# Optimization experiments

Measured on AMD Instinct MI355X. Metric: run time of the kernel, lower is better.

Reference implementation:

```python
import jax, jax.numpy as jnp
import numpy as np

LMAX, MMAX = 4, 2
L1 = LMAX + 1                      # 5 coefficients with m=0
NL = [LMAX + 1 - m for m in range(MMAX + 1)]   # [5,4,3] degrees per |m|
K = (LMAX + 1) ** 2                # 25 full SH coefficients
KR = NL[0] + 2 * sum(NL[1:])       # 19 coefficients with |m|<=mmax
# degree l of each row in the reduced (m-primary) layout:
# m=0: l=0..4 | m=+1: l=1..4 | m=-1: l=1..4 | m=+2: l=2..4 | m=-2: l=2..4
L_IDX = np.array([0,1,2,3,4, 1,2,3,4, 1,2,3,4, 2,3,4, 2,3,4])


def so2_conv(x, rad, w0, b0, wr1, wi1, wr2, wi2, c_out, extra):
    """SO(2)-equivariant conv over m-primary layout x: [E, KR, c_in].
    rad: optional per-edge radial weights [E, sum_m nl_m*c_in]."""
    E, _, c_in = x.shape
    # m = 0 block
    x0 = x[:, :L1].reshape(E, L1 * c_in)
    if rad is not None:
        x0 = x0 * rad[:, :L1 * c_in]
    y0 = x0 @ w0 + b0
    out0 = y0[:, :L1 * c_out].reshape(E, L1, c_out)
    gating = y0[:, L1 * c_out:] if extra else None
    outs = [out0]
    off_x, off_r = L1, L1 * c_in
    for nl, wr, wi in ((NL[1], wr1, wi1), (NL[2], wr2, wi2)):
        xr = x[:, off_x:off_x + nl].reshape(E, nl * c_in)
        xi = x[:, off_x + nl:off_x + 2 * nl].reshape(E, nl * c_in)
        if rad is not None:
            rm = rad[:, off_r:off_r + nl * c_in]
            xr, xi = xr * rm, xi * rm
        yr = xr @ wr - xi @ wi   # complex-style SO2 mixing
        yi = xi @ wr + xr @ wi
        outs += [yr.reshape(E, nl, c_out), yi.reshape(E, nl, c_out)]
        off_x += 2 * nl
        off_r += nl * c_in
    return jnp.concatenate(outs, axis=1), gating


def gate_act(gating, x):
    """GateActivation: silu on l=0 scalars, sigmoid gates per degree l>=1."""
    E, _, H = x.shape
    g = jax.nn.sigmoid(gating).reshape(E, LMAX, H)
    g_ext = jnp.concatenate([jnp.ones((E, 1, H), x.dtype), g], axis=1)
    out = x * g_ext[:, L_IDX]           # l=0 row gated by 1, replaced below
    return out.at[:, 0].set(jax.nn.silu(x[:, 0]))


def setup_inputs() -> dict:
    key = jax.random.key(0)
    ks = jax.random.split(key, 32)
    E, N, C, H, D, RH = 50000, 2500, 64, 64, 128, 64
    c_in1 = 2 * C
    rad_dim = sum(nl * c_in1 for nl in NL)          # 1536
    extra = LMAX * H                                 # 256

    def w(k, shape):
        return jax.random.normal(k, shape, jnp.float32) / np.sqrt(shape[0])

    inp = {
        'node_feats': jax.random.normal(ks[0], (N, K, C), jnp.float32),
        'edge_embeds': jax.random.normal(ks[1], (E, D), jnp.float32),
        'wigner': jax.random.normal(ks[2], (E, KR, K), jnp.float32) / np.sqrt(K),
        'wigner_inv': jax.random.normal(ks[3], (E, K, KR), jnp.float32) / np.sqrt(KR),
        'edge_envelope': jax.random.uniform(ks[4], (E, 1, 1), jnp.float32),
        'rad_w1': w(ks[5], (D, RH)), 'rad_b1': jnp.zeros((RH,), jnp.float32),
        'rad_w2': w(ks[6], (RH, rad_dim)), 'rad_b2': jnp.zeros((rad_dim,), jnp.float32),
        'w1_m0': w(ks[7], (L1 * c_in1, L1 * H + extra)),
        'b1_m0': jnp.zeros((L1 * H + extra,), jnp.float32),
        'w1_r1': w(ks[8], (NL[1] * c_in1, NL[1] * H)),
        'w1_i1': w(ks[9], (NL[1] * c_in1, NL[1] * H)),
        'w1_r2': w(ks[10], (NL[2] * c_in1, NL[2] * H)),
        'w1_i2': w(ks[11], (NL[2] * c_in1, NL[2] * H)),
        'w2_m0': w(ks[12], (L1 * H, L1 * C)),
        'b2_m0': jnp.zeros((L1 * C,), jnp.float32),
        'w2_r1': w(ks[13], (NL[1] * H, NL[1] * C)),
        'w2_i1': w(ks[14], (NL[1] * H, NL[1] * C)),
        'w2_r2': w(ks[15], (NL[2] * H, NL[2] * C)),
        'w2_i2': w(ks[16], (NL[2] * H, NL[2] * C)),
        'senders': jax.random.randint(ks[17], (E,), 0, N, jnp.int32),
        'receivers': jax.random.randint(ks[18], (E,), 0, N, jnp.int32),
    }
    return inp


def reference(node_feats, edge_embeds, wigner, wigner_inv, edge_envelope,
              rad_w1, rad_b1, rad_w2, rad_b2,
              w1_m0, b1_m0, w1_r1, w1_i1, w1_r2, w1_i2,
              w2_m0, b2_m0, w2_r1, w2_i1, w2_r2, w2_i2,
              senders, receivers):
    num_nodes = node_feats.shape[0]
    C = node_feats.shape[2]
    H = w2_m0.shape[0] // L1
    # gather + concat: [E, K, 2C]
    msg = jnp.concatenate((node_feats[senders], node_feats[receivers]), axis=2)
    # rotate to edge frame, truncated to |m|<=mmax: [E, KR, 2C]
    msg = jnp.einsum('erk,ekc->erc', wigner, msg)
    # per-edge radial weights for conv1
    rad = jax.nn.silu(edge_embeds @ rad_w1 + rad_b1) @ rad_w2 + rad_b2
    msg, gating = so2_conv(msg, rad, w1_m0, b1_m0, w1_r1, w1_i1, w1_r2, w1_i2,
                           c_out=H, extra=LMAX * H)
    msg = gate_act(gating, msg)
    msg, _ = so2_conv(msg, None, w2_m0, b2_m0, w2_r1, w2_i1, w2_r2, w2_i2,
                      c_out=C, extra=0)
    msg = msg * edge_envelope
    # rotate back to global frame: [E, K, C]
    msg = jnp.einsum('ekr,erc->ekc', wigner_inv, msg)
    return jax.ops.segment_sum(msg, receivers, num_segments=num_nodes)
```

## Files before the change

kernel.cpp:

```cpp
#include <hip/hip_runtime.h>


typedef __attribute__((ext_vector_type(8))) short bf16x8;
typedef __attribute__((ext_vector_type(4))) float f32x4;

union U8 { uint4 v; unsigned short s[8]; };

__device__ __forceinline__ unsigned short f2b(float f) {
    unsigned u = __float_as_uint(f);
    unsigned r = (u + 0x7FFFu + ((u >> 16) & 1u)) >> 16;
    return (unsigned short)r;
}
__device__ __forceinline__ float b2f(unsigned short h) {
    return __uint_as_float(((unsigned)h) << 16);
}
__device__ __forceinline__ float sigm_(float x){ return 1.0f/(1.0f+__expf(-x)); }
__device__ __forceinline__ float silu_(float x){ return x/(1.0f+__expf(-x)); }

#define OFF_W1T   0L
#define OFF_W1C1  409600L
#define OFF_W1C2  933888L
#define OFF_V0T   1327104L
#define OFF_V1C   1449984L
#define OFF_V2C   1712128L
#define OFF_RW2T  1908736L
#define W_TOTAL   2007040L
#define NNODES    2500
#define NFT_ELEMS (2500L * 2048L)

__global__ void k_prep(const float* __restrict__ w1m0, const float* __restrict__ w1r1,
                       const float* __restrict__ w1i1, const float* __restrict__ w1r2,
                       const float* __restrict__ w1i2, const float* __restrict__ w2m0,
                       const float* __restrict__ w2r1, const float* __restrict__ w2i1,
                       const float* __restrict__ w2r2, const float* __restrict__ w2i2,
                       const float* __restrict__ rw2, short* __restrict__ W)
{
    long i = (long)blockIdx.x * blockDim.x + threadIdx.x;
    if (i >= W_TOTAL) return;
    float v;
    if (i < OFF_W1C1) {
        int n = (int)(i / 640), k = (int)(i % 640);
        v = (n < 576) ? w1m0[k * 576 + n] : 0.f;
    } else if (i < OFF_W1C2) {
        long j = i - OFF_W1C1; int n = (int)(j >> 10), k = (int)(j & 1023);
        v = (n < 256) ? ((k < 512) ? w1r1[k*256 + n] : -w1i1[(k-512)*256 + n])
                      : ((k < 512) ? w1i1[k*256 + (n-256)] : w1r1[(k-512)*256 + (n-256)]);
    } else if (i < OFF_V0T) {
        long j = i - OFF_W1C2; int n = (int)(j / 768), k = (int)(j % 768);
        v = (n >= 384) ? 0.f
          : (n < 192) ? ((k < 384) ? w1r2[k*192 + n] : -w1i2[(k-384)*192 + n])
                      : ((k < 384) ? w1i2[k*192 + (n-192)] : w1r2[(k-384)*192 + (n-192)]);
    } else if (i < OFF_V1C) {
        long j = i - OFF_V0T; int n = (int)(j / 320), k = (int)(j % 320);
        v = (n < 320) ? w2m0[k * 320 + n] : 0.f;
    } else if (i < OFF_V2C) {
        long j = i - OFF_V1C; int n = (int)(j >> 9), k = (int)(j & 511);
        v = (n < 256) ? ((k < 256) ? w2r1[k*256 + n] : -w2i1[(k-256)*256 + n])
                      : ((k < 256) ? w2i1[k*256 + (n-256)] : w2r1[(k-256)*256 + (n-256)]);
    } else if (i < OFF_RW2T) {
        long j = i - OFF_V2C; int n = (int)(j / 384), k = (int)(j % 384);
        v = (n >= 384) ? 0.f
          : (n < 192) ? ((k < 192) ? w2r2[k*192 + n] : -w2i2[(k-192)*192 + n])
                      : ((k < 192) ? w2i2[k*192 + (n-192)] : w2r2[(k-192)*192 + (n-192)]);
    } else {
        long j = i - OFF_RW2T; int n = (int)(j >> 6), d = (int)(j & 63);
        v = rw2[d * 1536 + n];
    }
    W[i] = (short)f2b(v);
}

__global__ __launch_bounds__(256)
void k_nft(const float* __restrict__ nf, short* __restrict__ nfT)
{
    __shared__ float s_nf[25 * 65];
    const int t = threadIdx.x;
    const long nn = blockIdx.x;
    for (int p = t; p < 1600; p += 256) {
        int r = p >> 6, c = p & 63;
        s_nf[r * 65 + c] = nf[nn * 1600 + p];
    }
    __syncthreads();
    for (int i = t; i < 2048; i += 256) {
        int c = i >> 5, k = i & 31;
        float v = (k < 25) ? s_nf[k * 65 + c] : 0.f;
        nfT[nn * 2048 + i] = (short)f2b(v);
    }
}

__global__ void k_hist(const int* __restrict__ rcv, int* __restrict__ cnt, long e0, long n)
{
    long e = (long)blockIdx.x * 256 + threadIdx.x;
    if (e < n) atomicAdd(&cnt[rcv[e0 + e]], 1);
}

__global__ __launch_bounds__(256)
void k_scan(const int* __restrict__ cnt, int* __restrict__ off, int* __restrict__ nxt)
{
    __shared__ int part[256];
    const int t = threadIdx.x;
    const int base = t * 10;
    int loc[10]; int s = 0;
    #pragma unroll
    for (int j = 0; j < 10; ++j) {
        int idx = base + j;
        int v = (idx < NNODES) ? cnt[idx] : 0;
        loc[j] = s; s += v;
    }
    part[t] = s;
    __syncthreads();
    for (int d = 1; d < 256; d <<= 1) {
        int v = part[t];
        int u = (t >= d) ? part[t - d] : 0;
        __syncthreads();
        part[t] = v + u;
        __syncthreads();
    }
    int excl = (t == 0) ? 0 : part[t - 1];
    #pragma unroll
    for (int j = 0; j < 10; ++j) {
        int idx = base + j;
        if (idx < NNODES) { int o = excl + loc[j]; off[idx] = o; nxt[idx] = o; }
    }
}

__global__ void k_scat(const int* __restrict__ rcv, int* __restrict__ nxt,
                       int* __restrict__ perm, long e0, long n)
{
    long e = (long)blockIdx.x * 256 + threadIdx.x;
    if (e < n) {
        int p = atomicAdd(&nxt[rcv[e0 + e]], 1);
        perm[p] = (int)e;
    }
}

__global__ __launch_bounds__(512)
void k_rad(const float* __restrict__ ee, const float* __restrict__ rw1,
           const float* __restrict__ rb1, const float* __restrict__ rb2,
           const short* __restrict__ RW2T, short* __restrict__ rad,
           long e0, long Etot)
{
    __shared__ __align__(16) short s_h[32 * 64];
    const int t = threadIdx.x, w = t >> 6, l = t & 63, l15 = l & 15, lhi = l >> 4;
    const long eb = (long)blockIdx.x * 32;

    #pragma unroll
    for (int j = 0; j < 4; ++j) {
        int i = t + j * 512;
        int e = i >> 6, d = i & 63;
        long ge = e0 + eb + e;
        float a = rb1[d];
        if (ge < Etot) {
            const float* ep = ee + ge * 128;
            #pragma unroll 16
            for (int dd = 0; dd < 128; ++dd) a = fmaf(ep[dd], rw1[dd * 64 + d], a);
            a = silu_(a);
        } else a = 0.f;
        *(short*)((char*)s_h + e * 128 + ((d * 2) ^ ((e & 7) << 4))) = (short)f2b(a);
    }
    __syncthreads();

    f32x4 acc[6][2][2];
    #pragma unroll
    for (int g = 0; g < 6; ++g)
        #pragma unroll
        for (int mt = 0; mt < 2; ++mt)
            #pragma unroll
            for (int nt = 0; nt < 2; ++nt)
                acc[g][mt][nt] = (f32x4){0.f, 0.f, 0.f, 0.f};

    #pragma unroll
    for (int ks = 0; ks < 2; ++ks) {
        bf16x8 af[2];
        #pragma unroll
        for (int mt = 0; mt < 2; ++mt)
            af[mt] = *(const bf16x8*)((const char*)s_h + (mt * 16 + l15) * 128 +
                                      (((ks << 6) + (lhi << 4)) ^ ((l & 7) << 4)));
        #pragma unroll
        for (int g = 0; g < 6; ++g) {
            int grp = w + g * 8;
            #pragma unroll
            for (int nt = 0; nt < 2; ++nt) {
                int col = grp * 32 + nt * 16 + l15;
                bf16x8 bf = *(const bf16x8*)(RW2T + (long)col * 64 + (ks << 5) + (lhi << 3));
                #pragma unroll
                for (int mt = 0; mt < 2; ++mt)
                    acc[g][mt][nt] = __builtin_amdgcn_mfma_f32_16x16x32_bf16(af[mt], bf, acc[g][mt][nt], 0, 0, 0);
            }
        }
    }
    #pragma unroll
    for (int g = 0; g < 6; ++g)
        #pragma unroll
        for (int nt = 0; nt < 2; ++nt) {
            int col = (w + g * 8) * 32 + nt * 16 + l15;
            float bias = rb2[col];
            #pragma unroll
            for (int mt = 0; mt < 2; ++mt)
                #pragma unroll
                for (int r = 0; r < 4; ++r) {
                    int e = mt * 16 + lhi * 4 + r;
                    rad[(eb + e) * 1536 + col] = (short)f2b(acc[g][mt][nt][r] + bias);
                }
        }
}

__global__ __launch_bounds__(256)
void k_rot2(const float* __restrict__ wig, const short* __restrict__ nfT,
            const short* __restrict__ rad,
            const int* __restrict__ snd, const int* __restrict__ rcv,
            short* __restrict__ X, long e0, long nchunk)
{
    __shared__ float s_wg[4][480];
    __shared__ __align__(16) short s_rot[4][20 * 128];
    const int t = threadIdx.x, w = t >> 6, l = t & 63, l15 = l & 15, lhi = l >> 4;
    const long eb = (long)blockIdx.x * 4;
    const long el = eb + w;
    const bool valid = (el < nchunk);

    for (int p = t; p < 4 * 475; p += 256) {
        int e = p / 475, q = p - e * 475;
        if (eb + e < nchunk) s_wg[e][q] = wig[(e0 + eb + e) * 475 + q];
    }
    __syncthreads();

    if (valid) {
        long ge = e0 + el;
        int n0 = snd[ge], n1 = rcv[ge];
        U8 a0u, a1u;
        #pragma unroll
        for (int j = 0; j < 8; ++j) {
            int k = lhi * 8 + j;
            a0u.s[j] = (k < 25) ? f2b(s_wg[w][l15 * 25 + k]) : (unsigned short)0;
            a1u.s[j] = (l15 < 3 && k < 25) ? f2b(s_wg[w][(16 + l15) * 25 + k]) : (unsigned short)0;
        }
        bf16x8 a0 = *(bf16x8*)&a0u, a1 = *(bf16x8*)&a1u;

        f32x4 acc0[8], acc1[8];
        #pragma unroll
        for (int nt = 0; nt < 8; ++nt) {
            acc0[nt] = (f32x4){0.f, 0.f, 0.f, 0.f};
            acc1[nt] = (f32x4){0.f, 0.f, 0.f, 0.f};
        }
        #pragma unroll
        for (int nt = 0; nt < 8; ++nt) {
            int col = nt * 16 + l15;
            bf16x8 b = *(const bf16x8*)(nfT + (long)(col < 64 ? n0 : n1) * 2048 +
                                        (long)(col & 63) * 32 + (lhi << 3));
            acc0[nt] = __builtin_amdgcn_mfma_f32_16x16x32_bf16(a0, b, acc0[nt], 0, 0, 0);
            acc1[nt] = __builtin_amdgcn_mfma_f32_16x16x32_bf16(a1, b, acc1[nt], 0, 0, 0);
        }
        char* base = (char*)s_rot[w];
        #pragma unroll
        for (int nt = 0; nt < 8; ++nt) {
            int col2 = (nt * 16 + l15) * 2;
            #pragma unroll
            for (int r = 0; r < 4; ++r) {
                int row = lhi * 4 + r;
                *(short*)(base + ((row * 256 + col2) ^ ((row & 7) << 4))) = (short)f2b(acc0[nt][r]);
            }
            if (lhi == 0) {
                #pragma unroll
                for (int r = 0; r < 4; ++r) {
                    int row = 16 + r;
                    *(short*)(base + ((row * 256 + col2) ^ ((row & 7) << 4))) = (short)f2b(acc1[nt][r]);
                }
            }
        }
    }
    __syncthreads();

    short* xp = X + el * 2432;
    if (valid) {
        const short* rp = rad + el * 1536;
        #pragma unroll
        for (int it = 0; it < 5; ++it) {
            int q = l + it * 64;
            if (q < 304) {
                int r = q >> 4, c0 = (q & 15) << 3;
                int rr = (r < 9) ? r : ((r < 16) ? r - 4 : r - 7);
                U8 rot; rot.v = *(uint4*)((char*)s_rot[w] + ((r * 256 + c0 * 2) ^ ((r & 7) << 4)));
                U8 rd;  rd.v  = *(const uint4*)(rp + rr * 128 + c0);
                U8 o;
                #pragma unroll
                for (int j = 0; j < 8; ++j) o.s[j] = f2b(b2f(rot.s[j]) * b2f(rd.s[j]));
                *(uint4*)(xp + q * 8) = o.v;
            }
        }
    } else {
        #pragma unroll
        for (int it = 0; it < 5; ++it) {
            int q = l + it * 64;
            if (q < 304) *(uint4*)(xp + q * 8) = (uint4){0, 0, 0, 0};
        }
    }
}

template<int Km, int Nreal, int GMODE, int EPI>
__device__ __forceinline__ void gemm_body(
    const short* __restrict__ A, const long RS, const int gofs,
    const short* __restrict__ W, const float* __restrict__ bias,
    short* __restrict__ O, const long OS, const int oofs,
    short* __restrict__ sA, short* __restrict__ sB, const int et, const int cb)
{
    const int t = threadIdx.x, w = t >> 6, l = t & 63, l15 = l & 15, lhi = l >> 4;
    const long eb = (long)et * 128;
    const short* Ap = A + eb * RS;
    const short* Wp = W + (long)cb * Km;

    f32x4 acc[4][4];
    #pragma unroll
    for (int mt = 0; mt < 4; ++mt)
        #pragma unroll
        for (int nt = 0; nt < 4; ++nt)
            acc[mt][nt] = (f32x4){0.f, 0.f, 0.f, 0.f};

    int rowi[4], k8i[4];
    #pragma unroll
    for (int i = 0; i < 4; ++i) {
        int p = t + i * 256, frag = p >> 6, lif = p & 63;
        rowi[i] = ((frag >> 1) << 4) + (lif & 15);
        k8i[i]  = ((frag & 1) << 2) + (lif >> 4);
    }

    auto ldA = [&](int i, int kc) -> uint4 {
        const short* rp = Ap + (long)rowi[i] * RS;
        const int kg = kc + k8i[i] * 8;
        uint4 z = *(const uint4*)(rp + kg);
        if constexpr (GMODE == 0) return z;
        U8 zz; zz.v = z; U8 r;
        if constexpr (GMODE == 1) {
            int rr = kg >> 6;
            if (rr == 0) {
                #pragma unroll
                for (int q = 0; q < 8; ++q) r.s[q] = f2b(silu_(b2f(zz.s[q])));
            } else {
                U8 gg; gg.v = *(const uint4*)(rp + gofs + (rr - 1) * 64 + (kg & 63));
                #pragma unroll
                for (int q = 0; q < 8; ++q) r.s[q] = f2b(b2f(zz.s[q]) * b2f(gg.s[q]));
            }
        } else if constexpr (GMODE == 2) {
            U8 gg; gg.v = *(const uint4*)(rp + gofs + (kg & 255));
            #pragma unroll
            for (int q = 0; q < 8; ++q) r.s[q] = f2b(b2f(zz.s[q]) * b2f(gg.s[q]));
        } else {
            int gi = 64 + kg - ((kg >= 192) ? 192 : 0);
            U8 gg; gg.v = *(const uint4*)(rp + gofs + gi);
            #pragma unroll
            for (int q = 0; q < 8; ++q) r.s[q] = f2b(b2f(zz.s[q]) * b2f(gg.s[q]));
        }
        return r.v;
    };
    auto ldB = [&](int i, int kc) -> uint4 {
        return *(const uint4*)(Wp + (long)rowi[i] * Km + kc + k8i[i] * 8);
    };

    constexpr int NCH = Km / 64;
    uint4 rA[4], rB[4];
    #pragma unroll
    for (int i = 0; i < 4; ++i) { rA[i] = ldA(i, 0); rB[i] = ldB(i, 0); }

    for (int ch = 0; ch < NCH; ++ch) {
        __syncthreads();
        #pragma unroll
        for (int i = 0; i < 4; ++i) {
            *(uint4*)(sA + (t + i * 256) * 8) = rA[i];
            *(uint4*)(sB + (t + i * 256) * 8) = rB[i];
        }
        __syncthreads();
        if (ch + 1 < NCH) {
            #pragma unroll
            for (int i = 0; i < 4; ++i) {
                rA[i] = ldA(i, (ch + 1) * 64);
                rB[i] = ldB(i, (ch + 1) * 64);
            }
        }
        #pragma unroll
        for (int ks = 0; ks < 2; ++ks) {
            bf16x8 af[4], bf[4];
            #pragma unroll
            for (int mt = 0; mt < 4; ++mt)
                af[mt] = *(const bf16x8*)(sA + ((((w & 1) * 4 + mt) * 2 + ks) * 64 + l) * 8);
            #pragma unroll
            for (int nt = 0; nt < 4; ++nt)
                bf[nt] = *(const bf16x8*)(sB + ((((w >> 1) * 4 + nt) * 2 + ks) * 64 + l) * 8);
            #pragma unroll
            for (int mt = 0; mt < 4; ++mt)
                #pragma unroll
                for (int nt = 0; nt < 4; ++nt)
                    acc[mt][nt] = __builtin_amdgcn_mfma_f32_16x16x32_bf16(af[mt], bf[nt], acc[mt][nt], 0, 0, 0);
        }
    }

    const int r0 = (w & 1) * 64, c0 = (w >> 1) * 64;
    #pragma unroll
    for (int nt = 0; nt < 4; ++nt) {
        int jj = cb + c0 + nt * 16 + l15;
        if (jj < Nreal) {
            float b = (EPI >= 1) ? bias[jj] : 0.f;
            #pragma unroll
            for (int mt = 0; mt < 4; ++mt)
                #pragma unroll
                for (int r = 0; r < 4; ++r) {
                    long e = eb + r0 + mt * 16 + lhi * 4 + r;
                    float v = acc[mt][nt][r] + b;
                    if constexpr (EPI == 2) {
                        if (jj < 320) O[e * OS + jj] = (short)f2b(v);
                        else          O[e * OS + 1216 + (jj - 320)] = (short)f2b(sigm_(v));
                    } else {
                        O[e * OS + oofs + jj] = (short)f2b(v);
                    }
                }
        }
    }
}

__global__ __launch_bounds__(256)
void k_conv1(const short* __restrict__ X, const short* __restrict__ W0,
             const short* __restrict__ W1, const short* __restrict__ W2,
             const float* __restrict__ b1m0, short* __restrict__ Zr, int nbt)
{
    __shared__ __align__(16) short sA[8192];
    __shared__ __align__(16) short sB[8192];
    const int bid = blockIdx.x;
    const int s = bid >> 3;
    const int et = (bid & 7) + ((s / 13) << 3);
    const int ph = s % 13;
    if (et >= nbt) return;
    if (ph < 5)
        gemm_body< 640, 576, 0, 2>(X,        2432, 0, W0, b1m0,   Zr, 1536, 0,   sA, sB, et, ph << 7);
    else if (ph < 9)
        gemm_body<1024, 512, 0, 0>(X + 640,  2432, 0, W1, nullptr, Zr, 1536, 320, sA, sB, et, (ph - 5) << 7);
    else
        gemm_body< 768, 384, 0, 0>(X + 1664, 2432, 0, W2, nullptr, Zr, 1536, 832, sA, sB, et, (ph - 9) << 7);
}

__global__ __launch_bounds__(256)
void k_conv2(const short* __restrict__ Zr, const short* __restrict__ V0,
             const short* __restrict__ V1, const short* __restrict__ V2,
             const float* __restrict__ b2m0, short* __restrict__ Y2, int nbt)
{
    __shared__ __align__(16) short sA[8192];
    __shared__ __align__(16) short sB[8192];
    const int bid = blockIdx.x;
    const int s = bid >> 3;
    const int et = (bid & 7) + ((s / 11) << 3);
    const int ph = s % 11;
    if (et >= nbt) return;
    if (ph < 3)
        gemm_body<320, 320, 1, 1>(Zr,       1536, 1216, V0, b2m0,   Y2, 1216, 0,   sA, sB, et, ph << 7);
    else if (ph < 7)
        gemm_body<512, 512, 2, 0>(Zr + 320, 1536, 896,  V1, nullptr, Y2, 1216, 320, sA, sB, et, (ph - 3) << 7);
    else
        gemm_body<384, 384, 3, 0>(Zr + 832, 1536, 384,  V2, nullptr, Y2, 1216, 832, sA, sB, et, (ph - 7) << 7);
}

__global__ __launch_bounds__(256)
void k_invn(const short* __restrict__ Y2, const float* __restrict__ winv,
            const float* __restrict__ env, const int* __restrict__ cnt,
            const int* __restrict__ off, const int* __restrict__ perm,
            float* __restrict__ out, long e0)
{
    __shared__ __align__(16) short s_y[2][1216];
    __shared__ float s_wv[2][476];
    const int t = threadIdx.x;
    const int n = blockIdx.x;
    const int deg = cnt[n], start = off[n];

    float acc[7];
    #pragma unroll
    for (int j = 0; j < 7; ++j) acc[j] = 0.f;

    auto stage = [&](int i, int b) {
        int el = perm[start + i];
        long ge = e0 + el;
        if (t < 152) ((uint4*)s_y[b])[t] = *(const uint4*)(Y2 + (long)el * 1216 + t * 8);
        for (int p = t; p < 475; p += 256) s_wv[b][p] = winv[ge * 475 + p];
        if (t == 0) s_wv[b][475] = env[ge];
    };

    if (deg > 0) stage(0, 0);
    for (int i = 0; i < deg; ++i) {
        __syncthreads();
        if (i + 1 < deg) stage(i + 1, (i + 1) & 1);
        const short* sy = s_y[i & 1];
        const float* sw = s_wv[i & 1];
        float ev = sw[475];
        #pragma unroll
        for (int j = 0; j < 7; ++j) {
            int f = t + j * 256;
            if (f < 1600) {
                int r = f >> 6, c = f & 63;
                float a = 0.f;
                #pragma unroll
                for (int k = 0; k < 19; ++k)
                    a = fmaf(sw[r * 19 + k], b2f((unsigned short)sy[k * 64 + c]), a);
                acc[j] = fmaf(a, ev, acc[j]);
            }
        }
    }
    #pragma unroll
    for (int j = 0; j < 7; ++j) {
        int f = t + j * 256;
        if (f < 1600) out[(long)n * 1600 + f] += acc[j];
    }
}

extern "C" void kernel_launch(void* const* d_in, const int* in_sizes, int n_in,
                              void* d_out, int out_size, void* d_ws, size_t ws_size,
                              hipStream_t stream)
{
    const float* nf   = (const float*)d_in[0];
    const float* ee   = (const float*)d_in[1];
    const float* wig  = (const float*)d_in[2];
    const float* winv = (const float*)d_in[3];
    const float* env  = (const float*)d_in[4];
    const float* rw1  = (const float*)d_in[5];
    const float* rb1  = (const float*)d_in[6];
    const float* rw2  = (const float*)d_in[7];
    const float* rb2  = (const float*)d_in[8];
    const float* w1m0 = (const float*)d_in[9];
    const float* b1m0 = (const float*)d_in[10];
    const float* w1r1 = (const float*)d_in[11];
    const float* w1i1 = (const float*)d_in[12];
    const float* w1r2 = (const float*)d_in[13];
    const float* w1i2 = (const float*)d_in[14];
    const float* w2m0 = (const float*)d_in[15];
    const float* b2m0 = (const float*)d_in[16];
    const float* w2r1 = (const float*)d_in[17];
    const float* w2i1 = (const float*)d_in[18];
    const float* w2r2 = (const float*)d_in[19];
    const float* w2i2 = (const float*)d_in[20];
    const int*   snd  = (const int*)d_in[21];
    const int*   rcv  = (const int*)d_in[22];
    float* out = (float*)d_out;

    const long E = in_sizes[21];

    short* Wb  = (short*)d_ws;
    short* nfT = Wb + W_TOTAL;
    int* cnt   = (int*)(nfT + NFT_ELEMS);
    int* off   = cnt + 2512;
    int* nxt   = off + 2512;
    int* perm  = nxt + 2512;

    const size_t fixed = (size_t)W_TOTAL * 2 + (size_t)NFT_ELEMS * 2 + 3 * 2512 * 4;
    long cap = (ws_size > fixed) ? (long)((ws_size - fixed) / 7940) : 128;
    long chunk = (cap / 128) * 128;
    if (chunk < 128) chunk = 128;
    long Epad = ((E + 127) / 128) * 128;
    if (chunk > Epad) chunk = Epad;

    short* Xc = (short*)(perm + chunk);
    short* Rc = Xc + chunk * 2432;

    hipMemsetAsync(d_out, 0, (size_t)out_size * sizeof(float), stream);
    k_prep<<<(int)((W_TOTAL + 511) / 512), 512, 0, stream>>>(
        w1m0, w1r1, w1i1, w1r2, w1i2, w2m0, w2r1, w2i1, w2r2, w2i2, rw2, Wb);
    k_nft<<<NNODES, 256, 0, stream>>>(nf, nfT);

    for (long base = 0; base < E; base += chunk) {
        long n = E - base; if (n > chunk) n = chunk;
        int nb2 = (int)((n + 127) / 128);
        int nb8 = ((nb2 + 7) / 8) * 8;
        int nbe = (int)((n + 255) / 256);

        hipMemsetAsync(cnt, 0, NNODES * sizeof(int), stream);
        k_hist<<<nbe, 256, 0, stream>>>(rcv, cnt, base, n);
        k_scan<<<1, 256, 0, stream>>>(cnt, off, nxt);
        k_scat<<<nbe, 256, 0, stream>>>(rcv, nxt, perm, base, n);

        k_rad <<<(int)((n + 31) / 32), 512, 0, stream>>>(ee, rw1, rb1, rb2, Wb + OFF_RW2T, Rc, base, E);
        k_rot2<<<nb2 * 32, 256, 0, stream>>>(wig, nfT, Rc, snd, rcv, Xc, base, n);

        k_conv1<<<nb8 * 13, 256, 0, stream>>>(Xc, Wb + OFF_W1T, Wb + OFF_W1C1, Wb + OFF_W1C2, b1m0, Rc, nb2);
        k_conv2<<<nb8 * 11, 256, 0, stream>>>(Rc, Wb + OFF_V0T, Wb + OFF_V1C, Wb + OFF_V2C, b2m0, Xc, nb2);

        k_invn<<<NNODES, 256, 0, stream>>>(Xc, winv, env, cnt, off, perm, out, base);
    }
    (void)n_in;
}
```

Baseline: 1.211 ms.

## Split gating into standalone kernel and stage GEMM tiles via global_load_lds

Moves the gate activation (silu and sigmoid-gate multiplies) out of the conv2 GEMM A-load path into a separate elementwise kernel that rewrites Zr in place. Both GEMMs now copy A and B tiles straight from global memory into LDS with global_load_lds, replacing the register-staged prefetch of the next chunk. This simplifies the load path and lets the hardware's direct-to-LDS copy be used. In exchange it adds an extra read-write pass over Zr and drops the software overlap of next-chunk loads with MFMA work, since each chunk's loads now sit between two barriers.

```diff
diff --git a/kernel.cpp b/kernel.cpp
--- a/kernel.cpp
+++ b/kernel.cpp
@@ -16,6 +16,12 @@
 }
 __device__ __forceinline__ float sigm_(float x){ return 1.0f/(1.0f+__expf(-x)); }
 __device__ __forceinline__ float silu_(float x){ return x/(1.0f+__expf(-x)); }
+
+__device__ __forceinline__ void async16(short* lds, const short* g) {
+    __builtin_amdgcn_global_load_lds(
+        (const __attribute__((address_space(1))) void*)g,
+        (__attribute__((address_space(3))) void*)lds, 16, 0, 0);
+}
 
 #define OFF_W1T   0L
 #define OFF_W1C1  409600L
@@ -295,9 +301,43 @@
     }
 }
 
-template<int Km, int Nreal, int GMODE, int EPI>
+__global__ __launch_bounds__(256)
+void k_gate(short* __restrict__ Zr, long nitems)
+{
+    long idx = (long)blockIdx.x * 256 + threadIdx.x;
+    if (idx >= nitems) return;
+    long e = idx / 152;
+    int jg = (int)(idx - e * 152);
+    int j = jg * 8;
+    short* rp = Zr + e * 1536;
+    U8 z; z.v = *(const uint4*)(rp + j);
+    U8 o;
+    if (j < 320) {
+        int rr = j >> 6;
+        if (rr == 0) {
+            #pragma unroll
+            for (int q = 0; q < 8; ++q) o.s[q] = f2b(silu_(b2f(z.s[q])));
+        } else {
+            U8 g; g.v = *(const uint4*)(rp + 1216 + (rr - 1) * 64 + (j & 63));
+            #pragma unroll
+            for (int q = 0; q < 8; ++q) o.s[q] = f2b(b2f(z.s[q]) * b2f(g.s[q]));
+        }
+    } else if (j < 832) {
+        U8 g; g.v = *(const uint4*)(rp + 1216 + ((j - 320) & 255));
+        #pragma unroll
+        for (int q = 0; q < 8; ++q) o.s[q] = f2b(b2f(z.s[q]) * b2f(g.s[q]));
+    } else {
+        int gi = j - 832; if (gi >= 192) gi -= 192;
+        U8 g; g.v = *(const uint4*)(rp + 1280 + gi);
+        #pragma unroll
+        for (int q = 0; q < 8; ++q) o.s[q] = f2b(b2f(z.s[q]) * b2f(g.s[q]));
+    }
+    *(uint4*)(rp + j) = o.v;
+}
+
+template<int Km, int Nreal, int EPI>
 __device__ __forceinline__ void gemm_body(
-    const short* __restrict__ A, const long RS, const int gofs,
+    const short* __restrict__ A, const long RS,
     const short* __restrict__ W, const float* __restrict__ bias,
     short* __restrict__ O, const long OS, const int oofs,
     short* __restrict__ sA, short* __restrict__ sB, const int et, const int cb)
@@ -321,59 +361,18 @@
         rowi[i] = ((frag >> 1) << 4) + (lif & 15);
         k8i[i]  = ((frag & 1) << 2) + (lif >> 4);
     }
-
-    auto ldA = [&](int i, int kc) -> uint4 {
-        const short* rp = Ap + (long)rowi[i] * RS;
-        const int kg = kc + k8i[i] * 8;
-        uint4 z = *(const uint4*)(rp + kg);
-        if constexpr (GMODE == 0) return z;
-        U8 zz; zz.v = z; U8 r;
-        if constexpr (GMODE == 1) {
-            int rr = kg >> 6;
-            if (rr == 0) {
-                #pragma unroll
-                for (int q = 0; q < 8; ++q) r.s[q] = f2b(silu_(b2f(zz.s[q])));
-            } else {
-                U8 gg; gg.v = *(const uint4*)(rp + gofs + (rr - 1) * 64 + (kg & 63));
-                #pragma unroll
-                for (int q = 0; q < 8; ++q) r.s[q] = f2b(b2f(zz.s[q]) * b2f(gg.s[q]));
-            }
-        } else if constexpr (GMODE == 2) {
-            U8 gg; gg.v = *(const uint4*)(rp + gofs + (kg & 255));
-            #pragma unroll
-            for (int q = 0; q < 8; ++q) r.s[q] = f2b(b2f(zz.s[q]) * b2f(gg.s[q]));
-        } else {
-            int gi = 64 + kg - ((kg >= 192) ? 192 : 0);
-            U8 gg; gg.v = *(const uint4*)(rp + gofs + gi);
-            #pragma unroll
-            for (int q = 0; q < 8; ++q) r.s[q] = f2b(b2f(zz.s[q]) * b2f(gg.s[q]));
-        }
-        return r.v;
-    };
-    auto ldB = [&](int i, int kc) -> uint4 {
-        return *(const uint4*)(Wp + (long)rowi[i] * Km + kc + k8i[i] * 8);
-    };
+    const int wb = (t >> 6) << 6;
 
     constexpr int NCH = Km / 64;
-    uint4 rA[4], rB[4];
-    #pragma unroll
-    for (int i = 0; i < 4; ++i) { rA[i] = ldA(i, 0); rB[i] = ldB(i, 0); }
-
     for (int ch = 0; ch < NCH; ++ch) {
         __syncthreads();
+        const int kc = ch * 64;
         #pragma unroll
         for (int i = 0; i < 4; ++i) {
-            *(uint4*)(sA + (t + i * 256) * 8) = rA[i];
-            *(uint4*)(sB + (t + i * 256) * 8) = rB[i];
+            async16(sA + (wb + i * 256) * 8, Ap + (long)rowi[i] * RS + kc + k8i[i] * 8);
+            async16(sB + (wb + i * 256) * 8, Wp + (long)rowi[i] * Km + kc + k8i[i] * 8);
         }
         __syncthreads();
-        if (ch + 1 < NCH) {
-            #pragma unroll
-            for (int i = 0; i < 4; ++i) {
-                rA[i] = ldA(i, (ch + 1) * 64);
-                rB[i] = ldB(i, (ch + 1) * 64);
-            }
-        }
         #pragma unroll
         for (int ks = 0; ks < 2; ++ks) {
             bf16x8 af[4], bf[4];
@@ -427,11 +426,11 @@
     const int ph = s % 13;
     if (et >= nbt) return;
     if (ph < 5)
-        gemm_body< 640, 576, 0, 2>(X,        2432, 0, W0, b1m0,   Zr, 1536, 0,   sA, sB, et, ph << 7);
+        gemm_body< 640, 576, 2>(X,        2432, W0, b1m0,   Zr, 1536, 0,   sA, sB, et, ph << 7);
     else if (ph < 9)
-        gemm_body<1024, 512, 0, 0>(X + 640,  2432, 0, W1, nullptr, Zr, 1536, 320, sA, sB, et, (ph - 5) << 7);
+        gemm_body<1024, 512, 0>(X + 640,  2432, W1, nullptr, Zr, 1536, 320, sA, sB, et, (ph - 5) << 7);
     else
-        gemm_body< 768, 384, 0, 0>(X + 1664, 2432, 0, W2, nullptr, Zr, 1536, 832, sA, sB, et, (ph - 9) << 7);
+        gemm_body< 768, 384, 0>(X + 1664, 2432, W2, nullptr, Zr, 1536, 832, sA, sB, et, (ph - 9) << 7);
 }
 
 __global__ __launch_bounds__(256)
@@ -447,11 +446,11 @@
     const int ph = s % 11;
     if (et >= nbt) return;
     if (ph < 3)
-        gemm_body<320, 320, 1, 1>(Zr,       1536, 1216, V0, b2m0,   Y2, 1216, 0,   sA, sB, et, ph << 7);
+        gemm_body<320, 320, 1>(Zr,       1536, V0, b2m0,   Y2, 1216, 0,   sA, sB, et, ph << 7);
     else if (ph < 7)
-        gemm_body<512, 512, 2, 0>(Zr + 320, 1536, 896,  V1, nullptr, Y2, 1216, 320, sA, sB, et, (ph - 3) << 7);
+        gemm_body<512, 512, 0>(Zr + 320, 1536, V1, nullptr, Y2, 1216, 320, sA, sB, et, (ph - 3) << 7);
     else
-        gemm_body<384, 384, 3, 0>(Zr + 832, 1536, 384,  V2, nullptr, Y2, 1216, 832, sA, sB, et, (ph - 7) << 7);
+        gemm_body<384, 384, 0>(Zr + 832, 1536, V2, nullptr, Y2, 1216, 832, sA, sB, et, (ph - 7) << 7);
 }
 
 __global__ __launch_bounds__(256)
@@ -573,6 +572,10 @@
         k_rot2<<<nb2 * 32, 256, 0, stream>>>(wig, nfT, Rc, snd, rcv, Xc, base, n);
 
         k_conv1<<<nb8 * 13, 256, 0, stream>>>(Xc, Wb + OFF_W1T, Wb + OFF_W1C1, Wb + OFF_W1C2, b1m0, Rc, nb2);
+
+        long nitems = (long)nb2 * 128 * 152;
+        k_gate<<<(int)((nitems + 255) / 256), 256, 0, stream>>>(Rc, nitems);
+
         k_conv2<<<nb8 * 11, 256, 0, stream>>>(Rc, Wb + OFF_V0T, Wb + OFF_V1C, Wb + OFF_V2C, b2m0, Xc, nb2);
 
         k_invn<<<NNODES, 256, 0, stream>>>(Xc, winv, env, cnt, off, perm, out, base);
```

Result: faster. 1.176 ms (-2.9%).
